# Kernel optimization log

Hardware: AMD Instinct MI355X
Metric: run time of the kernel (lower is better)

Reference implementation:

```python
import jax, jax.numpy as jnp
import numpy as np

K_SIZE = 5
N_HEAD = 4


def flow_to_grid(flow, k_size=K_SIZE):
    # flow: (n, 2, h, w) -> normalized sample coords vx, vy: (n, k^2, h, w)
    n, _, h, w = flow.shape
    pad = (k_size - 1) // 2
    gy, gx = jnp.meshgrid(jnp.arange(h, dtype=flow.dtype),
                          jnp.arange(w, dtype=flow.dtype), indexing='ij')
    shift = jnp.arange(k_size, dtype=flow.dtype) - pad
    sy, sx = jnp.meshgrid(shift, shift, indexing='ij')  # (k,k), 'ij' like torch
    sy = sy.reshape(-1, 1, 1)  # (k^2,1,1)
    sx = sx.reshape(-1, 1, 1)
    sample_x = gx[None] + sx  # (k^2,h,w)
    sample_y = gy[None] + sy
    vx = sample_x[None] + flow[:, 0][:, None]  # (n,k^2,h,w)
    vy = sample_y[None] + flow[:, 1][:, None]
    vx = 2.0 * vx / max(w - 1, 1) - 1.0
    vy = 2.0 * vy / max(h - 1, 1) - 1.0
    return vx, vy


def grid_sample_zeros(feat, gx, gy):
    # feat: (C,H,W); gx, gy: (K2,h,w) normalized in [-1,1]
    # bilinear, padding_mode='zeros', align_corners=True
    C, H, W = feat.shape
    x = (gx + 1.0) * 0.5 * (W - 1)
    y = (gy + 1.0) * 0.5 * (H - 1)
    x0 = jnp.floor(x)
    y0 = jnp.floor(y)
    wx = x - x0
    wy = y - y0

    def gather(xi, yi):
        inb = (xi >= 0) & (xi <= W - 1) & (yi >= 0) & (yi <= H - 1)
        xi_c = jnp.clip(xi, 0, W - 1).astype(jnp.int32)
        yi_c = jnp.clip(yi, 0, H - 1).astype(jnp.int32)
        val = feat[:, yi_c, xi_c]  # (C,K2,h,w)
        return val * inb.astype(feat.dtype)

    v00 = gather(x0, y0)
    v01 = gather(x0 + 1, y0)
    v10 = gather(x0, y0 + 1)
    v11 = gather(x0 + 1, y0 + 1)
    return (v00 * (1 - wx) * (1 - wy) + v01 * wx * (1 - wy)
            + v10 * (1 - wx) * wy + v11 * wx * wy)  # (C,K2,h,w)


def setup_inputs() -> dict:
    key = jax.random.key(0)
    ks = jax.random.split(key, 8)
    n, c, h, w = 4, 128, 64, 64
    scale = 1.0 / np.sqrt(c)
    return {
        'q': jax.random.normal(ks[0], (n, c, h, w), jnp.float32),
        'k': jax.random.normal(ks[1], (n, c, h, w), jnp.float32),
        'v': jax.random.normal(ks[2], (n, c, h, w), jnp.float32),
        'flow': jax.random.normal(ks[3], (n, 2, h, w), jnp.float32) * 4.0,
        'Wq': jax.random.normal(ks[4], (c, c), jnp.float32) * scale,
        'Wk': jax.random.normal(ks[5], (c, c), jnp.float32) * scale,
        'Wv': jax.random.normal(ks[6], (c, c), jnp.float32) * scale,
        'Wfc': jax.random.normal(ks[7], (c, c), jnp.float32) * scale,
    }


def reference(q, k, v, flow, Wq, Wk, Wv, Wfc):
    # 1x1 convs == channel matmuls
    qp = jnp.einsum('oc,nchw->nohw', Wq, q)
    kp = jnp.einsum('oc,nchw->nohw', Wk, k)
    vp = jnp.einsum('oc,nchw->nohw', Wv, v)

    vx, vy = flow_to_grid(flow, K_SIZE)  # (n,K2,h,w) each
    ksamp = jax.vmap(grid_sample_zeros)(kp, vx, vy)  # (n,C,K2,h,w)
    vsamp = jax.vmap(grid_sample_zeros)(vp, vx, vy)

    n, C, K2, h, w = ksamp.shape
    d = C // N_HEAD
    qh = qp.reshape(n, N_HEAD, d, h, w)
    kh = ksamp.reshape(n, N_HEAD, d, K2, h, w)
    vh = vsamp.reshape(n, N_HEAD, d, K2, h, w)

    logits = jnp.einsum('nhdyx,nhdkyx->nhkyx', qh / jnp.sqrt(jnp.float32(d)), kh)
    attn = jax.nn.softmax(logits, axis=2)  # softmax over the k^2 window
    out = jnp.einsum('nhkyx,nhdkyx->nhdyx', attn, vh)
    out = out.reshape(n, N_HEAD * d, h, w)
    out = jnp.einsum('oc,nchw->nohw', Wfc, out)
    return out, attn
```

## Files before the change

kernel.cpp:

```cpp
#include <hip/hip_runtime.h>

constexpr int NB = 4;
constexpr int CC = 128;
constexpr int HH = 64;
constexpr int WW = 64;
constexpr int HWp = HH * WW;
constexpr int NHEADS = 4;
constexpr int K2 = 25;

typedef unsigned int   uint32;
typedef unsigned short ushort16;
typedef __attribute__((ext_vector_type(8))) short bf16x8;
typedef __attribute__((ext_vector_type(4))) float f32x4;

__device__ __forceinline__ ushort16 f2bf(float x) {
    uint32 b = __float_as_uint(x);
    return (ushort16)((b + 0x7FFFu + ((b >> 16) & 1u)) >> 16);
}
__device__ __forceinline__ uint32 pack2(float lo, float hi) {
    return ((uint32)f2bf(hi) << 16) | (uint32)f2bf(lo);
}
__device__ __forceinline__ float bf_lo(uint32 u) { return __uint_as_float(u << 16); }
__device__ __forceinline__ float bf_hi(uint32 u) { return __uint_as_float(u & 0xFFFF0000u); }

__global__ __launch_bounds__(256) void wconv_kernel(
    const float* __restrict__ Wq, const float* __restrict__ Wk,
    const float* __restrict__ Wv, const float* __restrict__ Wfc,
    ushort16* __restrict__ wbf)
{
    int i = blockIdx.x * 256 + threadIdx.x;
    int m = i >> 12;
    int j = i & 4095;
    const float* s = (m == 0) ? Wq : ((m == 1) ? Wk : ((m == 2) ? Wv : Wfc));
    float4 f = reinterpret_cast<const float4*>(s)[j];
    uint32 w0 = pack2(f.x, f.y);
    uint32 w1 = pack2(f.z, f.w);
    uint32* d = reinterpret_cast<uint32*>(wbf + (size_t)m * 16384);
    d[j * 2]     = w0;
    d[j * 2 + 1] = w1;
}

__global__ __launch_bounds__(256) void proj_mfma(
    const float* __restrict__ q, const float* __restrict__ k, const float* __restrict__ v,
    const ushort16* __restrict__ wbf,
    ushort16* __restrict__ qp, ushort16* __restrict__ kp, ushort16* __restrict__ vp)
{
    __shared__ __align__(16) ushort16 lx[64 * 132];

    int blk = blockIdx.x;
    int p   = blk >> 8;
    int rem = blk & 255;
    int n   = rem >> 6;
    int pt  = rem & 63;
    int pix0 = pt * 64;

    const float*    X  = (p == 0) ? q  : ((p == 1) ? k  : v);
    ushort16*       O  = (p == 0) ? qp : ((p == 1) ? kp : vp);
    const ushort16* Wb = wbf + (size_t)p * 16384;
    const float*    Xb = X + (size_t)n * CC * HWp + pix0;

    int lane = threadIdx.x & 63;
    int cg   = threadIdx.x >> 6;

#pragma unroll
    for (int i = 0; i < 16; ++i) {
        int c0 = i * 8 + cg * 2;
        float a = Xb[c0 * HWp + lane];
        float b = Xb[(c0 + 1) * HWp + lane];
        *reinterpret_cast<uint32*>(&lx[lane * 132 + c0]) = pack2(a, b);
    }
    __syncthreads();

    int wid = threadIdx.x >> 6;
    int wr  = wid >> 1, wc = wid & 1;
    int p16 = lane & 15, kg = lane >> 4;

    f32x4 acc[4][2] = {};

#pragma unroll
    for (int k0 = 0; k0 < 128; k0 += 32) {
        bf16x8 A[4], B[2];
#pragma unroll
        for (int ai = 0; ai < 4; ++ai) {
            int o = wr * 64 + ai * 16 + p16;
            A[ai] = *reinterpret_cast<const bf16x8*>(&Wb[o * 128 + k0 + kg * 8]);
        }
#pragma unroll
        for (int bj = 0; bj < 2; ++bj) {
            int px = wc * 32 + bj * 16 + p16;
            const ushort16* sp = &lx[px * 132 + k0 + kg * 8];
            struct { unsigned long long lo, hi; } t;
            t.lo = *reinterpret_cast<const unsigned long long*>(sp);
            t.hi = *reinterpret_cast<const unsigned long long*>(sp + 4);
            B[bj] = __builtin_bit_cast(bf16x8, t);
        }
#pragma unroll
        for (int ai = 0; ai < 4; ++ai)
#pragma unroll
            for (int bj = 0; bj < 2; ++bj)
                acc[ai][bj] = __builtin_amdgcn_mfma_f32_16x16x32_bf16(
                    A[ai], B[bj], acc[ai][bj], 0, 0, 0);
    }

    ushort16* Ob = O + (size_t)(n * HWp + pix0) * CC;
#pragma unroll
    for (int ai = 0; ai < 4; ++ai) {
        int ob = wr * 64 + ai * 16 + kg * 4;
#pragma unroll
        for (int bj = 0; bj < 2; ++bj) {
            int px = wc * 32 + bj * 16 + p16;
            uint32* dst = reinterpret_cast<uint32*>(&Ob[(size_t)px * CC + ob]);
            dst[0] = pack2(acc[ai][bj][0], acc[ai][bj][1]);
            dst[1] = pack2(acc[ai][bj][2], acc[ai][bj][3]);
        }
    }
}

__global__ __launch_bounds__(256) void attn_kernel(
    ushort16* qoh,
    const ushort16* __restrict__ kp, const ushort16* __restrict__ vp,
    const float* __restrict__ flow,
    float* __restrict__ attn)
{
    int blk = blockIdx.x;
    int swz = ((blk & 7) << 7) + (blk >> 3);
    int tid = threadIdx.x;
    int pix = swz * 16 + (tid >> 4);
    int lg  = tid & 15;
    int c0  = lg * 8;
    int n   = pix >> 12;
    int yx  = pix & 4095;
    int y   = yx >> 6, x = yx & 63;

    float fx = flow[((size_t)n * 2 + 0) * HWp + yx];
    float fy = flow[((size_t)n * 2 + 1) * HWp + yx];
    float pxf = (float)x + fx, pyf = (float)y + fy;
    float X0 = floorf(pxf), Y0 = floorf(pyf);
    float wx = pxf - X0,    wy = pyf - Y0;
    int ix0 = (int)X0 - 2,  iy0 = (int)Y0 - 2;

    int coff[6], roff[6];
    float mx[6], my[6];
#pragma unroll
    for (int r = 0; r < 6; ++r) {
        int xi = ix0 + r;
        mx[r] = (xi >= 0 && xi < WW) ? 1.f : 0.f;
        int xc = xi < 0 ? 0 : (xi > WW - 1 ? WW - 1 : xi);
        coff[r] = xc * CC;
        int yi = iy0 + r;
        my[r] = (yi >= 0 && yi < HH) ? 1.f : 0.f;
        int yc = yi < 0 ? 0 : (yi > HH - 1 ? HH - 1 : yi);
        roff[r] = yc * (WW * CC);
    }
    float wl[5], wr_[5], vt[5], vb2[5];
#pragma unroll
    for (int i = 0; i < 5; ++i) {
        wl[i]  = (1.f - wx) * mx[i];
        wr_[i] = wx * mx[i + 1];
        vt[i]  = (1.f - wy) * my[i];
        vb2[i] = wy * my[i + 1];
    }

    const ushort16* kb = kp + (size_t)n * HWp * CC + c0;
    const ushort16* vbp = vp + (size_t)n * HWp * CC + c0;
    ushort16* qb = qoh + (size_t)pix * CC + c0;

    uint4 qraw = *reinterpret_cast<const uint4*>(qb);
    float qv[8] = { bf_lo(qraw.x), bf_hi(qraw.x), bf_lo(qraw.y), bf_hi(qraw.y),
                    bf_lo(qraw.z), bf_hi(qraw.z), bf_lo(qraw.w), bf_hi(qraw.w) };

    float l[25];
#pragma unroll
    for (int r = 0; r < 6; ++r) {
        const ushort16* krow = kb + roff[r];
        float pd[6];
#pragma unroll
        for (int rx = 0; rx < 6; ++rx) {
            uint4 u = *reinterpret_cast<const uint4*>(krow + coff[rx]);
            float s = qv[0] * bf_lo(u.x) + qv[1] * bf_hi(u.x);
            s = fmaf(qv[2], bf_lo(u.y), s);
            s = fmaf(qv[3], bf_hi(u.y), s);
            s = fmaf(qv[4], bf_lo(u.z), s);
            s = fmaf(qv[5], bf_hi(u.z), s);
            s = fmaf(qv[6], bf_lo(u.w), s);
            s = fmaf(qv[7], bf_hi(u.w), s);
            pd[rx] = s;
        }
        float hbr[5];
#pragma unroll
        for (int kx = 0; kx < 5; ++kx)
            hbr[kx] = pd[kx] * wl[kx] + pd[kx + 1] * wr_[kx];
        if (r < 5) {
#pragma unroll
            for (int kx = 0; kx < 5; ++kx) l[r * 5 + kx] = hbr[kx] * vt[r];
        }
        if (r >= 1) {
#pragma unroll
            for (int kx = 0; kx < 5; ++kx)
                l[(r - 1) * 5 + kx] = fmaf(hbr[kx], vb2[r - 1], l[(r - 1) * 5 + kx]);
        }
    }

#pragma unroll
    for (int kk = 0; kk < 25; ++kk) {
        float s = l[kk];
        s += __shfl_xor(s, 1);
        s += __shfl_xor(s, 2);
        l[kk] = s * 0.17677669529663687f;
    }

    float m = l[0];
#pragma unroll
    for (int kk = 1; kk < 25; ++kk) m = fmaxf(m, l[kk]);
    float sum = 0.f;
#pragma unroll
    for (int kk = 0; kk < 25; ++kk) { l[kk] = __expf(l[kk] - m); sum += l[kk]; }
    float inv = 1.f / sum;
#pragma unroll
    for (int kk = 0; kk < 25; ++kk) l[kk] *= inv;

    {
        int head = lg >> 2, j = lg & 3;
        float* ab = attn + (((size_t)n * NHEADS + head) * K2) * HWp + yx;
#pragma unroll
        for (int kk = 0; kk < 25; ++kk)
            if ((kk & 3) == j) ab[(size_t)kk * HWp] = l[kk];
    }

    float acc[8] = {0.f, 0.f, 0.f, 0.f, 0.f, 0.f, 0.f, 0.f};
    float lhp[6] = {0.f, 0.f, 0.f, 0.f, 0.f, 0.f};
#pragma unroll
    for (int ry = 0; ry < 6; ++ry) {
        float lhc[6];
        if (ry < 5) {
            lhc[0] = l[ry * 5 + 0] * (1.f - wx);
#pragma unroll
            for (int rx = 1; rx < 5; ++rx)
                lhc[rx] = l[ry * 5 + rx] * (1.f - wx) + l[ry * 5 + rx - 1] * wx;
            lhc[5] = l[ry * 5 + 4] * wx;
        } else {
#pragma unroll
            for (int rx = 0; rx < 6; ++rx) lhc[rx] = 0.f;
        }
        float wyc = (1.f - wy) * my[ry];
        float wyp = wy * my[ry];
        const ushort16* vrow = vbp + roff[ry];
#pragma unroll
        for (int rx = 0; rx < 6; ++rx) {
            float w6 = (lhc[rx] * wyc + lhp[rx] * wyp) * mx[rx];
            uint4 u = *reinterpret_cast<const uint4*>(vrow + coff[rx]);
            acc[0] = fmaf(bf_lo(u.x), w6, acc[0]);
            acc[1] = fmaf(bf_hi(u.x), w6, acc[1]);
            acc[2] = fmaf(bf_lo(u.y), w6, acc[2]);
            acc[3] = fmaf(bf_hi(u.y), w6, acc[3]);
            acc[4] = fmaf(bf_lo(u.z), w6, acc[4]);
            acc[5] = fmaf(bf_hi(u.z), w6, acc[5]);
            acc[6] = fmaf(bf_lo(u.w), w6, acc[6]);
            acc[7] = fmaf(bf_hi(u.w), w6, acc[7]);
        }
#pragma unroll
        for (int rx = 0; rx < 6; ++rx) lhp[rx] = lhc[rx];
    }

    uint4 o;
    o.x = pack2(acc[0], acc[1]);
    o.y = pack2(acc[2], acc[3]);
    o.z = pack2(acc[4], acc[5]);
    o.w = pack2(acc[6], acc[7]);
    *reinterpret_cast<uint4*>(qb) = o;
}

__global__ __launch_bounds__(256) void fc_mfma(
    const ushort16* __restrict__ oh, const ushort16* __restrict__ wfcb,
    float* __restrict__ out)
{
    int blk = blockIdx.x;
    int gp0 = blk * 64;
    int n   = gp0 >> 12;
    int yx0 = gp0 & 4095;

    int lane = threadIdx.x & 63;
    int wid  = threadIdx.x >> 6;
    int wr = wid >> 1, wc = wid & 1;
    int p16 = lane & 15, kg = lane >> 4;

    const ushort16* ohb = oh + (size_t)gp0 * CC;

    f32x4 acc[4][2] = {};

#pragma unroll
    for (int k0 = 0; k0 < 128; k0 += 32) {
        bf16x8 A[4], B[2];
#pragma unroll
        for (int ai = 0; ai < 4; ++ai) {
            int o = wr * 64 + ai * 16 + p16;
            A[ai] = *reinterpret_cast<const bf16x8*>(&wfcb[o * 128 + k0 + kg * 8]);
        }
#pragma unroll
        for (int bj = 0; bj < 2; ++bj) {
            int px = wc * 32 + bj * 16 + p16;
            B[bj] = *reinterpret_cast<const bf16x8*>(&ohb[(size_t)px * CC + k0 + kg * 8]);
        }
#pragma unroll
        for (int ai = 0; ai < 4; ++ai)
#pragma unroll
            for (int bj = 0; bj < 2; ++bj)
                acc[ai][bj] = __builtin_amdgcn_mfma_f32_16x16x32_bf16(
                    A[ai], B[bj], acc[ai][bj], 0, 0, 0);
    }

    float* ob = out + (size_t)n * CC * HWp + yx0;
#pragma unroll
    for (int ai = 0; ai < 4; ++ai) {
        int o = wr * 64 + ai * 16 + kg * 4;
#pragma unroll
        for (int bj = 0; bj < 2; ++bj) {
            int px = wc * 32 + bj * 16 + p16;
#pragma unroll
            for (int r = 0; r < 4; ++r)
                ob[(size_t)(o + r) * HWp + px] = acc[ai][bj][r];
        }
    }
}

extern "C" void kernel_launch(void* const* d_in, const int* in_sizes, int n_in,
                              void* d_out, int out_size, void* d_ws, size_t ws_size,
                              hipStream_t stream)
{
    const float* q    = (const float*)d_in[0];
    const float* k    = (const float*)d_in[1];
    const float* v    = (const float*)d_in[2];
    const float* flow = (const float*)d_in[3];
    const float* Wq   = (const float*)d_in[4];
    const float* Wk   = (const float*)d_in[5];
    const float* Wv   = (const float*)d_in[6];
    const float* Wfc  = (const float*)d_in[7];

    float* out  = (float*)d_out;
    float* attn = out + (size_t)NB * CC * HWp;

    ushort16* ws = (ushort16*)d_ws;
    size_t slab = (size_t)NB * HWp * CC;
    ushort16* qp  = ws;
    ushort16* kp  = ws + slab;
    ushort16* vp  = ws + 2 * slab;
    ushort16* wbf = ws + 3 * slab;

    wconv_kernel<<<dim3(64), dim3(256), 0, stream>>>(Wq, Wk, Wv, Wfc, wbf);
    proj_mfma<<<dim3(768), dim3(256), 0, stream>>>(q, k, v, wbf, qp, kp, vp);
    attn_kernel<<<dim3(1024), dim3(256), 0, stream>>>(qp, kp, vp, flow, attn);
    fc_mfma<<<dim3(256), dim3(256), 0, stream>>>(qp, wbf + 3 * 16384, out);
}
```

Measured before the change: 49.60 us.

## Split attention kernel into separate QK-softmax and PV kernels

Splits the fused attention kernel into two launches. The first computes logits and softmax and writes the per-head attention weights as bf16 into the q buffer. The second reloads those weights, recomputes the sampling coordinates and accumulates V. The goal is lower register pressure per kernel and higher occupancy (launch bounds now 4 blocks per CU). The cost is an extra launch, a round trip of the weights through global memory, duplicated flow/offset arithmetic, and bf16 rounding of the attention weights before the V accumulation.

```diff
diff --git a/kernel.cpp b/kernel.cpp
--- a/kernel.cpp
+++ b/kernel.cpp
@@ -116,9 +116,9 @@
     }
 }
 
-__global__ __launch_bounds__(256) void attn_kernel(
-    ushort16* qoh,
-    const ushort16* __restrict__ kp, const ushort16* __restrict__ vp,
+__global__ __launch_bounds__(256, 4) void attn_qk(
+    ushort16* qrec,
+    const ushort16* __restrict__ kp,
     const float* __restrict__ flow,
     float* __restrict__ attn)
 {
@@ -161,13 +161,12 @@
         vb2[i] = wy * my[i + 1];
     }
 
-    const ushort16* kb = kp + (size_t)n * HWp * CC + c0;
-    const ushort16* vbp = vp + (size_t)n * HWp * CC + c0;
-    ushort16* qb = qoh + (size_t)pix * CC + c0;
-
+    ushort16* qb = qrec + (size_t)pix * CC + c0;
     uint4 qraw = *reinterpret_cast<const uint4*>(qb);
     float qv[8] = { bf_lo(qraw.x), bf_hi(qraw.x), bf_lo(qraw.y), bf_hi(qraw.y),
                     bf_lo(qraw.z), bf_hi(qraw.z), bf_lo(qraw.w), bf_hi(qraw.w) };
+
+    const ushort16* kb = kp + (size_t)n * HWp * CC + c0;
 
     float l[25];
 #pragma unroll
@@ -226,6 +225,81 @@
         for (int kk = 0; kk < 25; ++kk)
             if ((kk & 3) == j) ab[(size_t)kk * HWp] = l[kk];
     }
+
+    {
+        int j = lg & 3;
+        uint4 rec;
+        if (j == 0)
+            rec = make_uint4(pack2(l[0], l[1]),  pack2(l[2], l[3]),
+                             pack2(l[4], l[5]),  pack2(l[6], l[7]));
+        else if (j == 1)
+            rec = make_uint4(pack2(l[8], l[9]),  pack2(l[10], l[11]),
+                             pack2(l[12], l[13]), pack2(l[14], l[15]));
+        else if (j == 2)
+            rec = make_uint4(pack2(l[16], l[17]), pack2(l[18], l[19]),
+                             pack2(l[20], l[21]), pack2(l[22], l[23]));
+        else
+            rec = make_uint4(pack2(l[24], 0.f), 0u, 0u, 0u);
+        *reinterpret_cast<uint4*>(qb) = rec;
+    }
+}
+
+__global__ __launch_bounds__(256, 4) void attn_pv(
+    ushort16* rec_oh,
+    const ushort16* __restrict__ vp,
+    const float* __restrict__ flow)
+{
+    int blk = blockIdx.x;
+    int swz = ((blk & 7) << 7) + (blk >> 3);
+    int tid = threadIdx.x;
+    int pix = swz * 16 + (tid >> 4);
+    int lg  = tid & 15;
+    int c0  = lg * 8;
+    int n   = pix >> 12;
+    int yx  = pix & 4095;
+    int y   = yx >> 6, x = yx & 63;
+    int head = lg >> 2;
+
+    const uint4* rb = reinterpret_cast<const uint4*>(
+        rec_oh + (size_t)pix * CC + head * 32);
+    uint4 u0 = rb[0], u1 = rb[1], u2 = rb[2], u3 = rb[3];
+    float l[25];
+    l[0]  = bf_lo(u0.x); l[1]  = bf_hi(u0.x);
+    l[2]  = bf_lo(u0.y); l[3]  = bf_hi(u0.y);
+    l[4]  = bf_lo(u0.z); l[5]  = bf_hi(u0.z);
+    l[6]  = bf_lo(u0.w); l[7]  = bf_hi(u0.w);
+    l[8]  = bf_lo(u1.x); l[9]  = bf_hi(u1.x);
+    l[10] = bf_lo(u1.y); l[11] = bf_hi(u1.y);
+    l[12] = bf_lo(u1.z); l[13] = bf_hi(u1.z);
+    l[14] = bf_lo(u1.w); l[15] = bf_hi(u1.w);
+    l[16] = bf_lo(u2.x); l[17] = bf_hi(u2.x);
+    l[18] = bf_lo(u2.y); l[19] = bf_hi(u2.y);
+    l[20] = bf_lo(u2.z); l[21] = bf_hi(u2.z);
+    l[22] = bf_lo(u2.w); l[23] = bf_hi(u2.w);
+    l[24] = bf_lo(u3.x);
+
+    float fx = flow[((size_t)n * 2 + 0) * HWp + yx];
+    float fy = flow[((size_t)n * 2 + 1) * HWp + yx];
+    float pxf = (float)x + fx, pyf = (float)y + fy;
+    float X0 = floorf(pxf), Y0 = floorf(pyf);
+    float wx = pxf - X0,    wy = pyf - Y0;
+    int ix0 = (int)X0 - 2,  iy0 = (int)Y0 - 2;
+
+    int coff[6], roff[6];
+    float mx[6], my[6];
+#pragma unroll
+    for (int r = 0; r < 6; ++r) {
+        int xi = ix0 + r;
+        mx[r] = (xi >= 0 && xi < WW) ? 1.f : 0.f;
+        int xc = xi < 0 ? 0 : (xi > WW - 1 ? WW - 1 : xi);
+        coff[r] = xc * CC;
+        int yi = iy0 + r;
+        my[r] = (yi >= 0 && yi < HH) ? 1.f : 0.f;
+        int yc = yi < 0 ? 0 : (yi > HH - 1 ? HH - 1 : yi);
+        roff[r] = yc * (WW * CC);
+    }
+
+    const ushort16* vbp = vp + (size_t)n * HWp * CC + c0;
 
     float acc[8] = {0.f, 0.f, 0.f, 0.f, 0.f, 0.f, 0.f, 0.f};
     float lhp[6] = {0.f, 0.f, 0.f, 0.f, 0.f, 0.f};
@@ -267,7 +341,7 @@
     o.y = pack2(acc[2], acc[3]);
     o.z = pack2(acc[4], acc[5]);
     o.w = pack2(acc[6], acc[7]);
-    *reinterpret_cast<uint4*>(qb) = o;
+    *reinterpret_cast<uint4*>(rec_oh + (size_t)pix * CC + c0) = o;
 }
 
 __global__ __launch_bounds__(256) void fc_mfma(
@@ -348,6 +422,7 @@
 
     wconv_kernel<<<dim3(64), dim3(256), 0, stream>>>(Wq, Wk, Wv, Wfc, wbf);
     proj_mfma<<<dim3(768), dim3(256), 0, stream>>>(q, k, v, wbf, qp, kp, vp);
-    attn_kernel<<<dim3(1024), dim3(256), 0, stream>>>(qp, kp, vp, flow, attn);
+    attn_qk<<<dim3(1024), dim3(256), 0, stream>>>(qp, kp, flow, attn);
+    attn_pv<<<dim3(1024), dim3(256), 0, stream>>>(qp, vp, flow);
     fc_mfma<<<dim3(256), dim3(256), 0, stream>>>(qp, wbf + 3 * 16384, out);
 }
```

Measured after the change: 159.1 us. 221% more time.
